# Optimization experiments

Hardware: AMD Instinct MI355X
Metric: run time of the kernel (lower is better)

## Reference

```python
import jax, jax.numpy as jnp
import numpy as np

B, N_UNITS, SEQ, H = 4, 1024, 2048, 8
D_HEAD = N_UNITS // H
SCALE = 1.0 / D_HEAD ** 0.5


def setup_inputs() -> dict:
    key = jax.random.key(0)
    k1, k2, k3 = jax.random.split(key, 3)
    x = jax.random.normal(k1, (B, N_UNITS, SEQ), dtype=jnp.float32)
    # conv1x1 weights, bias=False; scaled like typical init
    W_qkv = jax.random.normal(k2, (3 * N_UNITS, N_UNITS), dtype=jnp.float32) * (1.0 / N_UNITS ** 0.5)
    W_out = jax.random.normal(k3, (N_UNITS, N_UNITS), dtype=jnp.float32) * (1.0 / N_UNITS ** 0.5)
    return {"x": x, "W_qkv": W_qkv, "W_out": W_out}


def reference(x, W_qkv, W_out):
    # x: (B, n_units, S). Conv1x1 == per-position linear along channel dim.
    qkv = jnp.einsum('oc,bcs->bos', W_qkv, x)          # (B, 3*n_units, S)
    Q, K, V = jnp.split(qkv, 3, axis=1)                # each (B, n_units, S)
    # torch.chunk along channels into h heads == reshape (B, h, d_head, S)
    Q = Q.reshape(B, H, D_HEAD, SEQ)
    K = K.reshape(B, H, D_HEAD, SEQ)
    V = V.reshape(B, H, D_HEAD, SEQ)
    # scores: Q^T K * scale  (NO softmax in original module; mask unused)
    A = jnp.einsum('bhdq,bhdk->bhqk', Q, K) * SCALE    # (B, h, S, S)
    # aggregation: sum_k A[q,k] * V[d,k]  (original does broadcast mul+sum)
    C = jnp.einsum('bhqk,bhdk->bhdq', A, V)            # (B, h, d_head, S)
    C = C.reshape(B, N_UNITS, SEQ)
    out = jnp.einsum('oc,bcs->bos', W_out, C)          # (B, n_units, S)
    return out
```

## Files before the change

### kernel.cpp

```cpp
#include <hip/hip_runtime.h>
#include <hip/hip_bf16.h>
#include <stdint.h>

using bf16 = __hip_bfloat16;

typedef __bf16 bf16x8 __attribute__((ext_vector_type(8)));
typedef float  f32x4  __attribute__((ext_vector_type(4)));

constexpr int Bc = 4, Hh = 8, Dh = 128, S = 2048, Cn = 1024, O3 = 3072;
constexpr float SCALE = 0.08838834764831845f;

#define GLDS16(gp, lp)                                               \
  __builtin_amdgcn_global_load_lds(                                  \
      (const __attribute__((address_space(1))) void*)(gp),           \
      (__attribute__((address_space(3))) void*)(lp), 16, 0, 0)

#define WAITVM(N) asm volatile("s_waitcnt vmcnt(" #N ")" ::: "memory")
#define BAR()                                  \
  do {                                         \
    asm volatile("" ::: "memory");             \
    __builtin_amdgcn_s_barrier();              \
    asm volatile("" ::: "memory");             \
  } while (0)

__device__ __forceinline__ void gemm_bt_core(
    const bf16* __restrict__ Abase, int lda,
    const bf16* __restrict__ Bbase, int ldb,
    int kIters, f32x4 (&acc)[4][4])
{
  alignas(16) __shared__ bf16 As[128 * 32];
  alignas(16) __shared__ bf16 Bs[128 * 32];
  const int t    = threadIdx.x;
  const int lane = t & 63;
  const int quad = lane >> 4, r16 = lane & 15;
  const int wave = t >> 6;
  const int wm = (wave & 1) * 64, wn = (wave >> 1) * 64;
  const int lrow = lane >> 2;
  const int lk   = (lane & 3) * 8;

  const long aOff0 = (long)(wave * 32 + lrow) * lda + lk;
  const long aOff1 = aOff0 + 16l * lda;
  const long bOff0 = (long)(wave * 32 + lrow) * ldb + lk;
  const long bOff1 = bOff0 + 16l * ldb;
  bf16* aL0 = &As[(wave * 32) * 32];
  bf16* aL1 = &As[(wave * 32 + 16) * 32];
  bf16* bL0 = &Bs[(wave * 32) * 32];
  bf16* bL1 = &Bs[(wave * 32 + 16) * 32];

#pragma unroll
  for (int i = 0; i < 4; i++)
#pragma unroll
    for (int j = 0; j < 4; j++) acc[i][j] = {0.f, 0.f, 0.f, 0.f};

  for (int ks = 0; ks < kIters; ++ks) {
    const int k0 = ks * 32;
    __syncthreads();
    GLDS16(Abase + k0 + aOff0, aL0);
    GLDS16(Abase + k0 + aOff1, aL1);
    GLDS16(Bbase + k0 + bOff0, bL0);
    GLDS16(Bbase + k0 + bOff1, bL1);
    __syncthreads();
    bf16x8 af[4], bfr[4];
#pragma unroll
    for (int i = 0; i < 4; i++)
      af[i] = *(const bf16x8*)&As[(wm + i * 16 + r16) * 32 + quad * 8];
#pragma unroll
    for (int j = 0; j < 4; j++)
      bfr[j] = *(const bf16x8*)&Bs[(wn + j * 16 + r16) * 32 + quad * 8];
#pragma unroll
    for (int i = 0; i < 4; i++)
#pragma unroll
      for (int j = 0; j < 4; j++)
        acc[i][j] = __builtin_amdgcn_mfma_f32_16x16x32_bf16(af[i], bfr[j], acc[i][j], 0, 0, 0);
  }
}

__device__ __forceinline__ void store_bf16_tile(
    f32x4 (&acc)[4][4], bf16* __restrict__ Cp, int ldc)
{
  const int t = threadIdx.x;
  const int lane = t & 63;
  const int quad = lane >> 4, r16 = lane & 15;
  const int wave = t >> 6;
  const int wm = (wave & 1) * 64, wn = (wave >> 1) * 64;
#pragma unroll
  for (int i = 0; i < 4; i++)
#pragma unroll
    for (int j = 0; j < 4; j++)
#pragma unroll
      for (int r = 0; r < 4; r++) {
        const int row = wm + i * 16 + quad * 4 + r;
        const int col = wn + j * 16 + r16;
        Cp[(long)row * ldc + col] = __float2bfloat16(acc[i][j][r]);
      }
}

__device__ __forceinline__ void store_f32_tile(
    f32x4 (&acc)[4][4], float* __restrict__ Cp, int ldc)
{
  const int t = threadIdx.x;
  const int lane = t & 63;
  const int quad = lane >> 4, r16 = lane & 15;
  const int wave = t >> 6;
  const int wm = (wave & 1) * 64, wn = (wave >> 1) * 64;
#pragma unroll
  for (int i = 0; i < 4; i++)
#pragma unroll
    for (int j = 0; j < 4; j++)
#pragma unroll
      for (int r = 0; r < 4; r++) {
        const int row = wm + i * 16 + quad * 4 + r;
        const int col = wn + j * 16 + r16;
        Cp[(long)row * ldc + col] = acc[i][j][r];
      }
}

__global__ __launch_bounds__(512, 2) void k_gemm_kv8(
    const bf16* __restrict__ WkvB, const bf16* __restrict__ xT, bf16* __restrict__ KV)
{
  constexpr int NT = Cn / 32;
  alignas(16) __shared__ bf16 smem[4 * 16384];

  const int orig = blockIdx.x;
  const int swz  = (orig & 7) * 32 + (orig >> 3);
  const int mt = swz >> 5;
  const int nt = swz & 31;
  const int m0 = mt * 256;

  const int tid  = threadIdx.x;
  const int lane = tid & 63;
  const int w    = tid >> 6;
  const int quad = lane >> 4, r16 = lane & 15;
  const int wm = (w >> 2) * 128;
  const int wn = (w & 3) * 64;

  const int srow = w * 16 + (lane >> 2);
  const int cx   = (lane & 3) ^ ((lane >> 3) & 3);
  const bf16* Ag = WkvB + (long)(m0 + srow) * Cn + cx * 8;
  const bf16* Bg = xT + (long)((long)nt * 256 + srow) * Cn + cx * 8;
  const int ldsW = w * 512;

#define KV8_STAGE_A(tt)                                                   \
  do {                                                                    \
    const int k0_ = (tt) * 32, bb_ = ((tt) & 3) * 16384;                  \
    GLDS16(Ag + k0_,             &smem[bb_ + ldsW]);                      \
    GLDS16(Ag + 128l * Cn + k0_, &smem[bb_ + 4096 + ldsW]);               \
  } while (0)
#define KV8_STAGE_B(tt)                                                   \
  do {                                                                    \
    const int k0_ = (tt) * 32, bb_ = ((tt) & 3) * 16384;                  \
    GLDS16(Bg + k0_,             &smem[bb_ + 8192 + ldsW]);               \
    GLDS16(Bg + 128l * Cn + k0_, &smem[bb_ + 8192 + 4096 + ldsW]);        \
  } while (0)

  const int sc8 = (quad ^ ((r16 >> 1) & 3)) * 8;

  f32x4 acc[8][4];
#pragma unroll
  for (int m = 0; m < 8; m++)
#pragma unroll
    for (int n = 0; n < 4; n++) acc[m][n] = {0.f, 0.f, 0.f, 0.f};

  KV8_STAGE_A(0); KV8_STAGE_B(0);
  KV8_STAGE_A(1); KV8_STAGE_B(1);
  KV8_STAGE_A(2); KV8_STAGE_B(2);
  WAITVM(8);
  BAR();

  bf16x8 af0[4], bfr0[4], af1[4];
  {
    const bf16* Ab = &smem[0];
    const bf16* Bb = Ab + 8192;
#pragma unroll
    for (int n = 0; n < 4; n++)
      bfr0[n] = *(const bf16x8*)&Bb[(wn + n * 16 + r16) * 32 + sc8];
#pragma unroll
    for (int m = 0; m < 4; m++)
      af0[m] = *(const bf16x8*)&Ab[(wm + m * 16 + r16) * 32 + sc8];
  }

#pragma unroll 4
  for (int tt = 0; tt < NT; ++tt) {
    const bf16* Ab = &smem[(tt & 3) * 16384];

    BAR();
    if (tt + 3 < NT) { KV8_STAGE_A(tt + 3); KV8_STAGE_B(tt + 3); }
#pragma unroll
    for (int m = 0; m < 4; m++)
      af1[m] = *(const bf16x8*)&Ab[(wm + (m + 4) * 16 + r16) * 32 + sc8];
    __builtin_amdgcn_s_setprio(1);
#pragma unroll
    for (int m = 0; m < 4; m++)
#pragma unroll
      for (int n = 0; n < 4; n++)
        acc[m][n] = __builtin_amdgcn_mfma_f32_16x16x32_bf16(af0[m], bfr0[n], acc[m][n], 0, 0, 0);
    __builtin_amdgcn_s_setprio(0);

    if (tt <= NT - 4)      { WAITVM(8); }
    else if (tt == NT - 3) { WAITVM(4); }
    else if (tt == NT - 2) { WAITVM(0); }
    BAR();

    __builtin_amdgcn_s_setprio(1);
#pragma unroll
    for (int m = 0; m < 4; m++)
#pragma unroll
      for (int n = 0; n < 4; n++)
        acc[m + 4][n] = __builtin_amdgcn_mfma_f32_16x16x32_bf16(af1[m], bfr0[n], acc[m + 4][n], 0, 0, 0);
    __builtin_amdgcn_s_setprio(0);

    if (tt + 1 < NT) {
      const bf16* Ab2 = &smem[((tt + 1) & 3) * 16384];
      const bf16* Bb2 = Ab2 + 8192;
#pragma unroll
      for (int n = 0; n < 4; n++)
        bfr0[n] = *(const bf16x8*)&Bb2[(wn + n * 16 + r16) * 32 + sc8];
#pragma unroll
      for (int m = 0; m < 4; m++)
        af0[m] = *(const bf16x8*)&Ab2[(wm + m * 16 + r16) * 32 + sc8];
    }
  }

  bf16* Cp = KV + (long)(nt >> 3) * 2048 * S + (long)m0 * S + (nt & 7) * 256;
#pragma unroll
  for (int m = 0; m < 8; m++)
#pragma unroll
    for (int n = 0; n < 4; n++)
#pragma unroll
      for (int r = 0; r < 4; r++) {
        const int row = wm + m * 16 + quad * 4 + r;
        const int col = wn + n * 16 + r16;
        Cp[(long)row * S + col] = __float2bfloat16(acc[m][n][r]);
      }
#undef KV8_STAGE_A
#undef KV8_STAGE_B
}

__global__ __launch_bounds__(512, 2) void k_gemm_out8(
    const bf16* __restrict__ W3, const bf16* __restrict__ xT, float* __restrict__ out)
{
  constexpr int NT = Cn / 32;
  alignas(16) __shared__ bf16 smem[4 * 12288];

  const int orig = blockIdx.x;
  const int swz  = (orig & 7) * 32 + (orig >> 3);
  const int b  = swz >> 6;
  const int mt = (swz >> 3) & 7;
  const int nt = swz & 7;
  const int m0 = mt * 128, n0 = nt * 256;

  const int tid  = threadIdx.x;
  const int lane = tid & 63;
  const int w    = tid >> 6;
  const int quad = lane >> 4, r16 = lane & 15;
  const int wm = (w >> 2) * 64;
  const int wn = (w & 3) * 64;

  const int srow = w * 16 + (lane >> 2);
  const int cx   = (lane & 3) ^ ((lane >> 3) & 3);
  const bf16* Ag = W3 + (long)b * Cn * Cn + (long)(m0 + srow) * Cn + cx * 8;
  const bf16* Bg = xT + (long)b * S * Cn + (long)(n0 + srow) * Cn + cx * 8;
  const int ldsW = w * 512;

#define OUT_STAGE(tt)                                                     \
  do {                                                                    \
    const int k0_ = (tt) * 32, bb_ = ((tt) & 3) * 12288;                  \
    GLDS16(Ag + k0_,             &smem[bb_ + ldsW]);                      \
    GLDS16(Bg + k0_,             &smem[bb_ + 4096 + ldsW]);               \
    GLDS16(Bg + 128l * Cn + k0_, &smem[bb_ + 8192 + ldsW]);               \
  } while (0)

  const int sc8 = (quad ^ ((r16 >> 1) & 3)) * 8;

  f32x4 acc[4][4];
#pragma unroll
  for (int m = 0; m < 4; m++)
#pragma unroll
    for (int n = 0; n < 4; n++) acc[m][n] = {0.f, 0.f, 0.f, 0.f};

  OUT_STAGE(0); OUT_STAGE(1); OUT_STAGE(2);
  WAITVM(6);
  BAR();

  bf16x8 af0[2], bfr0[4], af1[2];
  {
    const bf16* Ab = &smem[0];
    const bf16* Bb = Ab + 4096;
#pragma unroll
    for (int n = 0; n < 4; n++)
      bfr0[n] = *(const bf16x8*)&Bb[(wn + n * 16 + r16) * 32 + sc8];
#pragma unroll
    for (int m = 0; m < 2; m++)
      af0[m] = *(const bf16x8*)&Ab[(wm + m * 16 + r16) * 32 + sc8];
  }

#pragma unroll 4
  for (int tt = 0; tt < NT; ++tt) {
    const bf16* Ab = &smem[(tt & 3) * 12288];

    BAR();
    if (tt + 3 < NT) OUT_STAGE(tt + 3);
#pragma unroll
    for (int m = 0; m < 2; m++)
      af1[m] = *(const bf16x8*)&Ab[(wm + (m + 2) * 16 + r16) * 32 + sc8];
    __builtin_amdgcn_s_setprio(1);
#pragma unroll
    for (int m = 0; m < 2; m++)
#pragma unroll
      for (int n = 0; n < 4; n++)
        acc[m][n] = __builtin_amdgcn_mfma_f32_16x16x32_bf16(af0[m], bfr0[n], acc[m][n], 0, 0, 0);
    __builtin_amdgcn_s_setprio(0);

    if (tt <= NT - 4)      { WAITVM(6); }
    else if (tt == NT - 3) { WAITVM(3); }
    else if (tt == NT - 2) { WAITVM(0); }
    BAR();

    __builtin_amdgcn_s_setprio(1);
#pragma unroll
    for (int m = 0; m < 2; m++)
#pragma unroll
      for (int n = 0; n < 4; n++)
        acc[m + 2][n] = __builtin_amdgcn_mfma_f32_16x16x32_bf16(af1[m], bfr0[n], acc[m + 2][n], 0, 0, 0);
    __builtin_amdgcn_s_setprio(0);

    if (tt + 1 < NT) {
      const bf16* Ab2 = &smem[((tt + 1) & 3) * 12288];
      const bf16* Bb2 = Ab2 + 4096;
#pragma unroll
      for (int n = 0; n < 4; n++)
        bfr0[n] = *(const bf16x8*)&Bb2[(wn + n * 16 + r16) * 32 + sc8];
#pragma unroll
      for (int m = 0; m < 2; m++)
        af0[m] = *(const bf16x8*)&Ab2[(wm + m * 16 + r16) * 32 + sc8];
    }
  }

  float* Cp = out + (long)b * Cn * S + (long)m0 * S + n0;
#pragma unroll
  for (int m = 0; m < 4; m++)
#pragma unroll
    for (int n = 0; n < 4; n++)
#pragma unroll
      for (int r = 0; r < 4; r++) {
        const int row = wm + m * 16 + quad * 4 + r;
        const int col = wn + n * 16 + r16;
        Cp[(long)row * S + col] = acc[m][n][r];
      }
#undef OUT_STAGE
}

__global__ __launch_bounds__(256) void k_cvt_w(
    const float* __restrict__ Wkv, const float* __restrict__ Wout,
    bf16* __restrict__ WkvB, bf16* __restrict__ WoutB)
{
  const long v = (long)blockIdx.x * 256 + threadIdx.x;
  const bool isK = v < 524288;
  const float4 f = isK ? ((const float4*)Wkv)[v] : ((const float4*)Wout)[v - 524288];
  bf16 tmp[4];
  tmp[0] = __float2bfloat16(f.x);
  tmp[1] = __float2bfloat16(f.y);
  tmp[2] = __float2bfloat16(f.z);
  tmp[3] = __float2bfloat16(f.w);
  ushort4 u = *(ushort4*)tmp;
  if (isK) ((ushort4*)WkvB)[v] = u;
  else     ((ushort4*)WoutB)[v - 524288] = u;
}

__global__ __launch_bounds__(256) void k_transpose_cvt(
    const float* __restrict__ in, bf16* __restrict__ out, long inZ, long outZ,
    int inld, int outld)
{
  __shared__ bf16 tile[32][33];
  const float* ip = in + (long)blockIdx.z * inZ;
  bf16* op = out + (long)blockIdx.z * outZ;
  const int c0 = blockIdx.x * 32, r0 = blockIdx.y * 32;
  const int tx = threadIdx.x & 31, ty = threadIdx.x >> 5;
#pragma unroll
  for (int i = 0; i < 32; i += 8)
    tile[ty + i][tx] = __float2bfloat16(ip[(long)(r0 + ty + i) * inld + c0 + tx]);
  __syncthreads();
#pragma unroll
  for (int i = 0; i < 32; i += 8)
    op[(long)(c0 + ty + i) * outld + r0 + tx] = tile[tx][ty + i];
}

__global__ __launch_bounds__(256) void k_gemm_mt(
    const bf16* __restrict__ KV, float* __restrict__ MTpart)
{
  const int chunk = blockIdx.x;
  const int z = blockIdx.y;
  const int b = z >> 3, h = z & 7;
  const bf16* base = KV + (long)b * 2048 * S;
  const bf16* A  = base + (long)(h * Dh) * S + chunk * 256;
  const bf16* Bp = base + (long)(1024 + h * Dh) * S + chunk * 256;
  f32x4 acc[4][4];
  gemm_bt_core(A, S, Bp, S, 8, acc);
  store_f32_tile(acc, MTpart + ((long)chunk * 32 + z) * (Dh * Dh), Dh);
}

__global__ __launch_bounds__(256) void k_reduce_mt(
    const float* __restrict__ MTpart, bf16* __restrict__ MbT)
{
  const long i = (long)blockIdx.x * 256 + threadIdx.x;
  float s = 0.f;
#pragma unroll
  for (int c = 0; c < 8; c++) s += MTpart[(long)c * 32 * Dh * Dh + i];
  MbT[i] = __float2bfloat16(s * SCALE);
}

__global__ __launch_bounds__(256) void k_gemm_w2(
    const bf16* __restrict__ WoutB, const bf16* __restrict__ MbT, bf16* __restrict__ W2)
{
  const int m0 = blockIdx.x * 128;
  const int h = blockIdx.y, b = blockIdx.z;
  const int z = b * 8 + h;
  f32x4 acc[4][4];
  gemm_bt_core(WoutB + (long)m0 * Cn + h * Dh, Cn,
               MbT + (long)z * Dh * Dh, Dh, 4, acc);
  store_bf16_tile(acc, W2 + (long)b * Cn * Cn + (long)m0 * Cn + h * Dh, Cn);
}

__global__ __launch_bounds__(256) void k_gemm_w3(
    const bf16* __restrict__ W2, const bf16* __restrict__ WqT, bf16* __restrict__ W3)
{
  const int m0 = blockIdx.x * 128, n0 = blockIdx.y * 128, b = blockIdx.z;
  f32x4 acc[4][4];
  gemm_bt_core(W2 + (long)b * Cn * Cn + (long)m0 * Cn, Cn,
               WqT + (long)n0 * Cn, Cn, Cn / 32, acc);
  store_bf16_tile(acc, W3 + (long)b * Cn * Cn + (long)m0 * Cn + n0, Cn);
}

extern "C" void kernel_launch(void* const* d_in, const int* in_sizes, int n_in,
                              void* d_out, int out_size, void* d_ws, size_t ws_size,
                              hipStream_t stream)
{
  const float* x    = (const float*)d_in[0];
  const float* Wqkv = (const float*)d_in[1];
  const float* Wout = (const float*)d_in[2];
  float* out = (float*)d_out;

  char* ws = (char*)d_ws;
  bf16*  KV     = (bf16*)ws;
  bf16*  xT     = (bf16*)(ws + 33554432);
  float* MTpart = (float*)(ws + 50331648);
  bf16*  W3     = (bf16*)(ws + 50331648);
  bf16*  WkvB   = (bf16*)(ws + 67108864);
  bf16*  WoutB  = (bf16*)(ws + 71303168);
  bf16*  WqT    = (bf16*)(ws + 73400320);
  bf16*  MbT    = (bf16*)(ws + 75497472);
  bf16*  W2     = (bf16*)(ws + 76546048);

  k_cvt_w<<<dim3(3072), 256, 0, stream>>>(Wqkv + (long)Cn * Cn, Wout, WkvB, WoutB);
  k_transpose_cvt<<<dim3(64, 32, 4), 256, 0, stream>>>(
      x, xT, (long)1024 * 2048, (long)2048 * 1024, 2048, 1024);
  k_transpose_cvt<<<dim3(32, 32, 1), 256, 0, stream>>>(
      Wqkv, WqT, 0, 0, 1024, 1024);
  k_gemm_kv8<<<dim3(256), 512, 0, stream>>>(WkvB, xT, KV);
  k_gemm_mt<<<dim3(8, 32), 256, 0, stream>>>(KV, MTpart);
  k_reduce_mt<<<dim3(2048), 256, 0, stream>>>(MTpart, MbT);
  k_gemm_w2<<<dim3(8, 8, 4), 256, 0, stream>>>(WoutB, MbT, W2);
  k_gemm_w3<<<dim3(8, 8, 4), 256, 0, stream>>>(W2, WqT, W3);
  k_gemm_out8<<<dim3(256), 512, 0, stream>>>(W3, xT, out);
}
```

Baseline: 202.9 us.

## Compute Q projection directly instead of folding Wq into the output weights

Drops the W3 = W2·Wq weight-folding GEMM and the separate transpose of Wq. A new pipelined bf16 MFMA kernel computes Q^T = x^T·Wq^T per batch, and the final GEMM multiplies W2 by Q^T. The weight conversion now covers all of Wqkv in one pass, and the block-to-tile mapping in the KV GEMM is changed. The intent is to remove the small-tile W3 GEMM and the transpose launch, at the cost of more total FLOPs (a full S×C×C GEMM per batch in place of the C×C×C fold) and an extra 16 MB bf16 intermediate written and read back.

```diff
diff --git a/kernel.cpp b/kernel.cpp
--- a/kernel.cpp
+++ b/kernel.cpp
@@ -122,9 +122,8 @@
   alignas(16) __shared__ bf16 smem[4 * 16384];
 
   const int orig = blockIdx.x;
-  const int swz  = (orig & 7) * 32 + (orig >> 3);
-  const int mt = swz >> 5;
-  const int nt = swz & 31;
+  const int mt = orig >> 5;
+  const int nt = ((orig & 7) << 2) | ((orig >> 3) & 3);
   const int m0 = mt * 256;
 
   const int tid  = threadIdx.x;
@@ -237,7 +236,7 @@
 }
 
 __global__ __launch_bounds__(512, 2) void k_gemm_out8(
-    const bf16* __restrict__ W3, const bf16* __restrict__ xT, float* __restrict__ out)
+    const bf16* __restrict__ W2, const bf16* __restrict__ QT, float* __restrict__ out)
 {
   constexpr int NT = Cn / 32;
   alignas(16) __shared__ bf16 smem[4 * 12288];
@@ -258,8 +257,8 @@
 
   const int srow = w * 16 + (lane >> 2);
   const int cx   = (lane & 3) ^ ((lane >> 3) & 3);
-  const bf16* Ag = W3 + (long)b * Cn * Cn + (long)(m0 + srow) * Cn + cx * 8;
-  const bf16* Bg = xT + (long)b * S * Cn + (long)(n0 + srow) * Cn + cx * 8;
+  const bf16* Ag = W2 + (long)b * Cn * Cn + (long)(m0 + srow) * Cn + cx * 8;
+  const bf16* Bg = QT + (long)b * S * Cn + (long)(n0 + srow) * Cn + cx * 8;
   const int ldsW = w * 512;
 
 #define OUT_STAGE(tt)                                                     \
@@ -350,26 +349,138 @@
 #undef OUT_STAGE
 }
 
+__global__ __launch_bounds__(512, 2) void k_gemm_qt8(
+    const bf16* __restrict__ xT, const bf16* __restrict__ WqB, bf16* __restrict__ QT)
+{
+  constexpr int NT = Cn / 32;
+  alignas(16) __shared__ bf16 smem[4 * 12288];
+
+  const int orig = blockIdx.x;
+  const int b  = orig >> 6;
+  const int mt = (orig >> 2) & 15;
+  const int nt = orig & 3;
+  const int m0 = mt * 128, n0 = nt * 256;
+
+  const int tid  = threadIdx.x;
+  const int lane = tid & 63;
+  const int w    = tid >> 6;
+  const int quad = lane >> 4, r16 = lane & 15;
+  const int wm = (w >> 2) * 64;
+  const int wn = (w & 3) * 64;
+
+  const int srow = w * 16 + (lane >> 2);
+  const int cx   = (lane & 3) ^ ((lane >> 3) & 3);
+  const bf16* Ag = xT + (long)b * S * Cn + (long)(m0 + srow) * Cn + cx * 8;
+  const bf16* Bg = WqB + (long)(n0 + srow) * Cn + cx * 8;
+  const int ldsW = w * 512;
+
+#define QT_STAGE(tt)                                                      \
+  do {                                                                    \
+    const int k0_ = (tt) * 32, bb_ = ((tt) & 3) * 12288;                  \
+    GLDS16(Ag + k0_,             &smem[bb_ + ldsW]);                      \
+    GLDS16(Bg + k0_,             &smem[bb_ + 4096 + ldsW]);               \
+    GLDS16(Bg + 128l * Cn + k0_, &smem[bb_ + 8192 + ldsW]);               \
+  } while (0)
+
+  const int sc8 = (quad ^ ((r16 >> 1) & 3)) * 8;
+
+  f32x4 acc[4][4];
+#pragma unroll
+  for (int m = 0; m < 4; m++)
+#pragma unroll
+    for (int n = 0; n < 4; n++) acc[m][n] = {0.f, 0.f, 0.f, 0.f};
+
+  QT_STAGE(0); QT_STAGE(1); QT_STAGE(2);
+  WAITVM(6);
+  BAR();
+
+  bf16x8 af0[2], bfr0[4], af1[2];
+  {
+    const bf16* Ab = &smem[0];
+    const bf16* Bb = Ab + 4096;
+#pragma unroll
+    for (int n = 0; n < 4; n++)
+      bfr0[n] = *(const bf16x8*)&Bb[(wn + n * 16 + r16) * 32 + sc8];
+#pragma unroll
+    for (int m = 0; m < 2; m++)
+      af0[m] = *(const bf16x8*)&Ab[(wm + m * 16 + r16) * 32 + sc8];
+  }
+
+#pragma unroll 4
+  for (int tt = 0; tt < NT; ++tt) {
+    const bf16* Ab = &smem[(tt & 3) * 12288];
+
+    BAR();
+    if (tt + 3 < NT) QT_STAGE(tt + 3);
+#pragma unroll
+    for (int m = 0; m < 2; m++)
+      af1[m] = *(const bf16x8*)&Ab[(wm + (m + 2) * 16 + r16) * 32 + sc8];
+    __builtin_amdgcn_s_setprio(1);
+#pragma unroll
+    for (int m = 0; m < 2; m++)
+#pragma unroll
+      for (int n = 0; n < 4; n++)
+        acc[m][n] = __builtin_amdgcn_mfma_f32_16x16x32_bf16(af0[m], bfr0[n], acc[m][n], 0, 0, 0);
+    __builtin_amdgcn_s_setprio(0);
+
+    if (tt <= NT - 4)      { WAITVM(6); }
+    else if (tt == NT - 3) { WAITVM(3); }
+    else if (tt == NT - 2) { WAITVM(0); }
+    BAR();
+
+    __builtin_amdgcn_s_setprio(1);
+#pragma unroll
+    for (int m = 0; m < 2; m++)
+#pragma unroll
+      for (int n = 0; n < 4; n++)
+        acc[m + 2][n] = __builtin_amdgcn_mfma_f32_16x16x32_bf16(af1[m], bfr0[n], acc[m + 2][n], 0, 0, 0);
+    __builtin_amdgcn_s_setprio(0);
+
+    if (tt + 1 < NT) {
+      const bf16* Ab2 = &smem[((tt + 1) & 3) * 12288];
+      const bf16* Bb2 = Ab2 + 4096;
+#pragma unroll
+      for (int n = 0; n < 4; n++)
+        bfr0[n] = *(const bf16x8*)&Bb2[(wn + n * 16 + r16) * 32 + sc8];
+#pragma unroll
+      for (int m = 0; m < 2; m++)
+        af0[m] = *(const bf16x8*)&Ab2[(wm + m * 16 + r16) * 32 + sc8];
+    }
+  }
+
+  bf16* Cp = QT + (long)b * S * Cn + (long)m0 * Cn + n0;
+#pragma unroll
+  for (int m = 0; m < 4; m++)
+#pragma unroll
+    for (int n = 0; n < 4; n++)
+#pragma unroll
+      for (int r = 0; r < 4; r++) {
+        const int row = wm + m * 16 + quad * 4 + r;
+        const int col = wn + n * 16 + r16;
+        Cp[(long)row * Cn + col] = __float2bfloat16(acc[m][n][r]);
+      }
+#undef QT_STAGE
+}
+
 __global__ __launch_bounds__(256) void k_cvt_w(
-    const float* __restrict__ Wkv, const float* __restrict__ Wout,
-    bf16* __restrict__ WkvB, bf16* __restrict__ WoutB)
+    const float* __restrict__ Wqkv, const float* __restrict__ Wout,
+    bf16* __restrict__ WqkvB, bf16* __restrict__ WoutB)
 {
   const long v = (long)blockIdx.x * 256 + threadIdx.x;
-  const bool isK = v < 524288;
-  const float4 f = isK ? ((const float4*)Wkv)[v] : ((const float4*)Wout)[v - 524288];
+  const bool isQ = v < 786432;
+  const float4 f = isQ ? ((const float4*)Wqkv)[v] : ((const float4*)Wout)[v - 786432];
   bf16 tmp[4];
   tmp[0] = __float2bfloat16(f.x);
   tmp[1] = __float2bfloat16(f.y);
   tmp[2] = __float2bfloat16(f.z);
   tmp[3] = __float2bfloat16(f.w);
   ushort4 u = *(ushort4*)tmp;
-  if (isK) ((ushort4*)WkvB)[v] = u;
-  else     ((ushort4*)WoutB)[v - 524288] = u;
+  if (isQ) ((ushort4*)WqkvB)[v] = u;
+  else     ((ushort4*)WoutB)[v - 786432] = u;
 }
 
 __global__ __launch_bounds__(256) void k_transpose_cvt(
-    const float* __restrict__ in, bf16* __restrict__ out, long inZ, long outZ,
-    int inld, int outld)
+    const float* __restrict__ in, bf16* __restrict__ out, long inZ, long outZ)
 {
   __shared__ bf16 tile[32][33];
   const float* ip = in + (long)blockIdx.z * inZ;
@@ -378,11 +489,11 @@
   const int tx = threadIdx.x & 31, ty = threadIdx.x >> 5;
 #pragma unroll
   for (int i = 0; i < 32; i += 8)
-    tile[ty + i][tx] = __float2bfloat16(ip[(long)(r0 + ty + i) * inld + c0 + tx]);
+    tile[ty + i][tx] = __float2bfloat16(ip[(long)(r0 + ty + i) * 2048 + c0 + tx]);
   __syncthreads();
 #pragma unroll
   for (int i = 0; i < 32; i += 8)
-    op[(long)(c0 + ty + i) * outld + r0 + tx] = tile[tx][ty + i];
+    op[(long)(c0 + ty + i) * 1024 + r0 + tx] = tile[tx][ty + i];
 }
 
 __global__ __launch_bounds__(256) void k_gemm_mt(
@@ -421,16 +532,6 @@
   store_bf16_tile(acc, W2 + (long)b * Cn * Cn + (long)m0 * Cn + h * Dh, Cn);
 }
 
-__global__ __launch_bounds__(256) void k_gemm_w3(
-    const bf16* __restrict__ W2, const bf16* __restrict__ WqT, bf16* __restrict__ W3)
-{
-  const int m0 = blockIdx.x * 128, n0 = blockIdx.y * 128, b = blockIdx.z;
-  f32x4 acc[4][4];
-  gemm_bt_core(W2 + (long)b * Cn * Cn + (long)m0 * Cn, Cn,
-               WqT + (long)n0 * Cn, Cn, Cn / 32, acc);
-  store_bf16_tile(acc, W3 + (long)b * Cn * Cn + (long)m0 * Cn + n0, Cn);
-}
-
 extern "C" void kernel_launch(void* const* d_in, const int* in_sizes, int n_in,
                               void* d_out, int out_size, void* d_ws, size_t ws_size,
                               hipStream_t stream)
@@ -444,22 +545,20 @@
   bf16*  KV     = (bf16*)ws;
   bf16*  xT     = (bf16*)(ws + 33554432);
   float* MTpart = (float*)(ws + 50331648);
-  bf16*  W3     = (bf16*)(ws + 50331648);
-  bf16*  WkvB   = (bf16*)(ws + 67108864);
-  bf16*  WoutB  = (bf16*)(ws + 71303168);
-  bf16*  WqT    = (bf16*)(ws + 73400320);
+  bf16*  QT     = (bf16*)(ws + 50331648);
+  bf16*  WqkvB  = (bf16*)(ws + 67108864);
+  bf16*  WoutB  = (bf16*)(ws + 73400320);
   bf16*  MbT    = (bf16*)(ws + 75497472);
   bf16*  W2     = (bf16*)(ws + 76546048);
-
-  k_cvt_w<<<dim3(3072), 256, 0, stream>>>(Wqkv + (long)Cn * Cn, Wout, WkvB, WoutB);
+  bf16*  WkvB   = WqkvB + (long)Cn * Cn;
+
+  k_cvt_w<<<dim3(4096), 256, 0, stream>>>(Wqkv, Wout, WqkvB, WoutB);
   k_transpose_cvt<<<dim3(64, 32, 4), 256, 0, stream>>>(
-      x, xT, (long)1024 * 2048, (long)2048 * 1024, 2048, 1024);
-  k_transpose_cvt<<<dim3(32, 32, 1), 256, 0, stream>>>(
-      Wqkv, WqT, 0, 0, 1024, 1024);
+      x, xT, (long)1024 * 2048, (long)2048 * 1024);
   k_gemm_kv8<<<dim3(256), 512, 0, stream>>>(WkvB, xT, KV);
   k_gemm_mt<<<dim3(8, 32), 256, 0, stream>>>(KV, MTpart);
   k_reduce_mt<<<dim3(2048), 256, 0, stream>>>(MTpart, MbT);
   k_gemm_w2<<<dim3(8, 8, 4), 256, 0, stream>>>(WoutB, MbT, W2);
-  k_gemm_w3<<<dim3(8, 8, 4), 256, 0, stream>>>(W2, WqT, W3);
-  k_gemm_out8<<<dim3(256), 512, 0, stream>>>(W3, xT, out);
-}
+  k_gemm_qt8<<<dim3(256), 512, 0, stream>>>(xT, WqkvB, QT);
+  k_gemm_out8<<<dim3(256), 512, 0, stream>>>(W2, QT, out);
+}
```

Result: faster. 197.8 us (-2.5%).
